# Kernel optimization log

Measured on AMD Instinct MI355X. Metric: run time of the kernel, lower is better.

## Reference

```python
import jax, jax.numpy as jnp
import numpy as np

TWO_PI = 6.283185307179586
ALPHA_CLIP = 0.999

def setup_inputs() -> dict:
    key = jax.random.key(0)
    k1, k2, k3, k4 = jax.random.split(key, 4)
    N, H, W = 256, 512, 512
    xyz = jax.random.uniform(k1, (N, 2), jnp.float32, -1.0, 1.0)      # NDC centers in [-1,1]
    rotation = jax.random.normal(k2, (N, 1), jnp.float32)             # pre-sigmoid angle
    scaling = jax.random.uniform(k3, (N, 2), jnp.float32, 0.05, 0.5)  # inverse std (init 1/5)
    features_dc = jax.random.uniform(k4, (N, 3), jnp.float32)         # RGB in [0,1]
    opacity = jnp.ones((N, 1), jnp.float32)                            # buffer of ones
    background = jnp.ones((3,), jnp.float32)                           # white background
    return {"xyz": xyz, "rotation": rotation, "scaling": scaling,
            "features_dc": features_dc, "opacity": opacity,
            "background": background, "H": H, "W": W}

def _render(xyz, rotation, scaling, features_dc, opacity, background, H, W):
    N = xyz.shape[0]
    # Project NDC [-1,1] -> pixel coords (x,y)
    wh = jnp.array([W, H], jnp.float32)
    means = (xyz * 0.5 + 0.5) * wh                                    # [N,2]
    # Anisotropic 2D covariance: std = 1/|scaling| px, angle via sigmoid
    theta = jax.nn.sigmoid(rotation[:, 0]) * TWO_PI                   # [N]
    std = 1.0 / (jnp.abs(scaling) + 1e-6)                             # [N,2]
    s0, s1 = std[:, 0] ** 2, std[:, 1] ** 2
    c, s = jnp.cos(theta), jnp.sin(theta)
    # Sigma = R diag(s0,s1) R^T
    A = c * c * s0 + s * s * s1
    B = c * s * (s0 - s1)
    Cc = s * s * s0 + c * c * s1
    det = A * Cc - B * B + 1e-12
    ia, ib, ic = Cc / det, -B / det, A / det                          # conic (inverse cov)
    # Pixel centers, flattened P = H*W
    px = jnp.arange(W, dtype=jnp.float32) + 0.5
    py = jnp.arange(H, dtype=jnp.float32) + 0.5
    gx, gy = jnp.meshgrid(px, py)                                     # [H,W]
    gx, gy = gx.reshape(-1), gy.reshape(-1)                           # [P]
    dx = gx[None, :] - means[:, 0:1]                                  # [N,P]
    dy = gy[None, :] - means[:, 1:2]                                  # [N,P]
    power = -0.5 * (ia[:, None] * dx * dx + 2.0 * ib[:, None] * dx * dy
                    + ic[:, None] * dy * dy)                          # [N,P] <= 0
    alpha = jnp.minimum(opacity * jnp.exp(power), ALPHA_CLIP)         # [N,P]
    # Front-to-back alpha compositing in gaussian index order
    logs = jnp.log1p(-alpha)                                          # [N,P]
    csum = jnp.cumsum(logs, axis=0)
    T_excl = jnp.exp(jnp.concatenate([jnp.zeros((1, alpha.shape[1]), alpha.dtype),
                                      csum[:-1]], axis=0))            # transmittance before i
    weights = alpha * T_excl                                          # [N,P]
    T_final = jnp.exp(csum[-1])                                       # [P]
    img = jnp.einsum('np,nc->cp', weights, features_dc)               # [3,P]
    img = img + background[:, None] * T_final[None, :]
    return img.reshape(3, H, W)

def reference(xyz, rotation, scaling, features_dc, opacity, background, H, W):
    return _render(xyz, rotation, scaling, features_dc, opacity, background, H, W)
```

## Files before the change

### kernel.cpp

```cpp
#include <hip/hip_runtime.h>
#include <math.h>


#define BLOCK 256
#define QMAX 30.0f
#define ALPHA_CLIP 0.999f
#define LOG2E 1.4426950408889634f

__global__ __launch_bounds__(BLOCK) void render_kernel(
    const float* __restrict__ xyz,
    const float* __restrict__ rot,
    const float* __restrict__ scal,
    const float* __restrict__ feat,
    const float* __restrict__ opac,
    const float* __restrict__ bg,
    const int* __restrict__ dH,
    const int* __restrict__ dW,
    float* __restrict__ out,
    int N, int P)
{
    __shared__ float sg[BLOCK * 16];
    __shared__ int   list[BLOCK];
    __shared__ int   wcnt[BLOCK / 64];
    __shared__ int   sM;

    const int t = threadIdx.x;
    const int W = *dW, H = *dH;
    const int tiles_x = W >> 6;
    const int tx0 = (blockIdx.x % tiles_x) << 6;
    const int ty0 = (blockIdx.x / tiles_x) << 4;

    const float fx0 = (float)tx0, fx1 = (float)(tx0 + 64);
    const float fy0 = (float)ty0, fy1 = (float)(ty0 + 16);

    const float gxp  = fx0 + (float)(t & 63) + 0.5f;
    const float gyp0 = fy0 + (float)(t >> 6) + 0.5f;

    float T[4]  = {1.f, 1.f, 1.f, 1.f};
    float ar[4] = {0.f, 0.f, 0.f, 0.f};
    float ag[4] = {0.f, 0.f, 0.f, 0.f};
    float ab[4] = {0.f, 0.f, 0.f, 0.f};

    for (int c0 = 0; c0 < N; c0 += BLOCK) {
        const int i = c0 + t;
        bool pred = false;
        if (i < N) {
            const float Wf = (float)W, Hf = (float)H;
            const float mx = (xyz[2*i]   * 0.5f + 0.5f) * Wf;
            const float my = (xyz[2*i+1] * 0.5f + 0.5f) * Hf;
            const float r  = rot[i];
            const float theta = (1.0f / (1.0f + expf(-r))) * 6.283185307179586f;
            const float sd0 = 1.0f / (fabsf(scal[2*i])   + 1e-6f);
            const float sd1 = 1.0f / (fabsf(scal[2*i+1]) + 1e-6f);
            const float s0 = sd0 * sd0, s1 = sd1 * sd1;
            const float c = cosf(theta), s = sinf(theta);
            const float A  = c*c*s0 + s*s*s1;
            const float B  = c*s*(s0 - s1);
            const float Cc = s*s*s0 + c*c*s1;
            const float det = A*Cc - B*B + 1e-12f;
            const float inv = 1.0f / det;
            const float kk = -0.5f * LOG2E;
            const float rx = sqrtf(QMAX * A);
            const float ry = sqrtf(QMAX * Cc);

            float* rec = &sg[t * 16];
            rec[0]  = mx;
            rec[1]  = my;
            rec[2]  = Cc * inv * kk;
            rec[3]  = -B * inv * 2.0f * kk;
            rec[4]  = A  * inv * kk;
            rec[5]  = log2f(opac[i]);
            rec[6]  = feat[3*i+0];
            rec[7]  = feat[3*i+1];
            rec[8]  = feat[3*i+2];
            rec[12] = mx - rx;
            rec[13] = mx + rx;
            rec[14] = my - ry;
            rec[15] = my + ry;

            pred = (rec[13] >= fx0) & (rec[12] <= fx1) &
                   (rec[15] >= fy0) & (rec[14] <= fy1);
        }

        const unsigned long long m = __ballot(pred);
        const int lane = t & 63, wid = t >> 6;
        if (lane == 0) wcnt[wid] = __popcll(m);
        __syncthreads();
        int off = 0;
        for (int w = 0; w < wid; ++w) off += wcnt[w];
        if (pred)
            list[off + __popcll(m & ((1ull << lane) - 1ull))] = t;
        if (t == 0) sM = wcnt[0] + wcnt[1] + wcnt[2] + wcnt[3];
        __syncthreads();
        const int M = sM;

        for (int j = 0; j < M; ++j) {
            const int idx = list[j];
            const float* rec = &sg[idx * 16];
            const float4 g0 = *(const float4*)rec;
            const float4 g1 = *(const float4*)(rec + 4);
            const float  cb = rec[8];
            const float dx = gxp - g0.x;
            const float q0 = fmaf(g0.z * dx, dx, g1.y);
            const float bx = g0.w * dx;
#pragma unroll
            for (int k = 0; k < 4; ++k) {
                const float dy = (gyp0 + 4.0f * (float)k) - g0.y;
                const float ea = fmaf(dy, fmaf(g1.x, dy, bx), q0);
                const float alpha = fminf(exp2f(ea), ALPHA_CLIP);
                const float w = alpha * T[k];
                ar[k] = fmaf(w, g1.z, ar[k]);
                ag[k] = fmaf(w, g1.w, ag[k]);
                ab[k] = fmaf(w, cb, ab[k]);
                T[k] -= w;
            }
        }
        __syncthreads();
    }

    const float b0 = bg[0], b1 = bg[1], b2 = bg[2];
    const int px = tx0 + (t & 63);
#pragma unroll
    for (int k = 0; k < 4; ++k) {
        const int py = ty0 + (t >> 6) + 4 * k;
        if (px < W && py < H) {
            const int p = py * W + px;
            out[p]         = fmaf(b0, T[k], ar[k]);
            out[P + p]     = fmaf(b1, T[k], ag[k]);
            out[2*P + p]   = fmaf(b2, T[k], ab[k]);
        }
    }
}

extern "C" void kernel_launch(void* const* d_in, const int* in_sizes, int n_in,
                              void* d_out, int out_size, void* d_ws, size_t ws_size,
                              hipStream_t stream) {
    const float* xyz  = (const float*)d_in[0];
    const float* rot  = (const float*)d_in[1];
    const float* scal = (const float*)d_in[2];
    const float* feat = (const float*)d_in[3];
    const float* opac = (const float*)d_in[4];
    const float* bg   = (const float*)d_in[5];
    const int*   dH   = (const int*)d_in[6];
    const int*   dW   = (const int*)d_in[7];
    float* out = (float*)d_out;

    const int N = in_sizes[0] / 2;
    const int P = out_size / 3;

    const int blocks = (P + 1023) / 1024;
    render_kernel<<<blocks, BLOCK, 0, stream>>>(xyz, rot, scal, feat, opac, bg,
                                                dH, dW, out, N, P);
}
```

Measured before the change: 72.26 us.

## Precompute gaussian records in a prep kernel and halve tile size

Moves per-gaussian parameter setup (sigmoid, sin/cos, conic, bounding box) into a separate prep kernel that writes 16-float records to workspace, so each render block only loads them with float4 reads instead of recomputing them. It also shrinks the pixel tile from 64x16 to 32x16, which doubles the block count and gives each thread 2 pixels instead of 4. The goal is less redundant transcendental math per block and more blocks to fill the GPU, at the cost of an extra kernel launch and less per-thread reuse of each gaussian load.

```diff
diff --git a/kernel.cpp b/kernel.cpp
--- a/kernel.cpp
+++ b/kernel.cpp
@@ -7,14 +7,53 @@
 #define ALPHA_CLIP 0.999f
 #define LOG2E 1.4426950408889634f
 
+__global__ void prep_kernel(const float* __restrict__ xyz,
+                            const float* __restrict__ rot,
+                            const float* __restrict__ scal,
+                            const float* __restrict__ feat,
+                            const float* __restrict__ opac,
+                            const int* __restrict__ dH,
+                            const int* __restrict__ dW,
+                            float* __restrict__ gp, int N) {
+    int i = blockIdx.x * blockDim.x + threadIdx.x;
+    if (i >= N) return;
+    const float Wf = (float)(*dW), Hf = (float)(*dH);
+    const float mx = (xyz[2*i]   * 0.5f + 0.5f) * Wf;
+    const float my = (xyz[2*i+1] * 0.5f + 0.5f) * Hf;
+    const float r  = rot[i];
+    const float theta = (1.0f / (1.0f + expf(-r))) * 6.283185307179586f;
+    const float sd0 = 1.0f / (fabsf(scal[2*i])   + 1e-6f);
+    const float sd1 = 1.0f / (fabsf(scal[2*i+1]) + 1e-6f);
+    const float s0 = sd0 * sd0, s1 = sd1 * sd1;
+    const float c = cosf(theta), s = sinf(theta);
+    const float A  = c*c*s0 + s*s*s1;
+    const float B  = c*s*(s0 - s1);
+    const float Cc = s*s*s0 + c*c*s1;
+    const float det = A*Cc - B*B + 1e-12f;
+    const float inv = 1.0f / det;
+    const float kk = -0.5f * LOG2E;
+    const float rx = sqrtf(QMAX * A);
+    const float ry = sqrtf(QMAX * Cc);
+    float* rec = &gp[i * 16];
+    rec[0]  = mx;
+    rec[1]  = my;
+    rec[2]  = Cc * inv * kk;
+    rec[3]  = -B * inv * 2.0f * kk;
+    rec[4]  = A  * inv * kk;
+    rec[5]  = log2f(opac[i]);
+    rec[6]  = feat[3*i+0];
+    rec[7]  = feat[3*i+1];
+    rec[8]  = feat[3*i+2];
+    rec[9]  = 0.f; rec[10] = 0.f; rec[11] = 0.f;
+    rec[12] = mx - rx;
+    rec[13] = mx + rx;
+    rec[14] = my - ry;
+    rec[15] = my + ry;
+}
+
 __global__ __launch_bounds__(BLOCK) void render_kernel(
-    const float* __restrict__ xyz,
-    const float* __restrict__ rot,
-    const float* __restrict__ scal,
-    const float* __restrict__ feat,
-    const float* __restrict__ opac,
+    const float* __restrict__ gp,
     const float* __restrict__ bg,
-    const int* __restrict__ dH,
     const int* __restrict__ dW,
     float* __restrict__ out,
     int N, int P)
@@ -25,61 +64,30 @@
     __shared__ int   sM;
 
     const int t = threadIdx.x;
-    const int W = *dW, H = *dH;
-    const int tiles_x = W >> 6;
-    const int tx0 = (blockIdx.x % tiles_x) << 6;
+    const int W = *dW;
+    const int tiles_x = W >> 5;
+    const int tx0 = (blockIdx.x % tiles_x) << 5;
     const int ty0 = (blockIdx.x / tiles_x) << 4;
 
-    const float fx0 = (float)tx0, fx1 = (float)(tx0 + 64);
+    const float fx0 = (float)tx0, fx1 = (float)(tx0 + 32);
     const float fy0 = (float)ty0, fy1 = (float)(ty0 + 16);
 
-    const float gxp  = fx0 + (float)(t & 63) + 0.5f;
-    const float gyp0 = fy0 + (float)(t >> 6) + 0.5f;
+    const float gxp  = fx0 + (float)(t & 31) + 0.5f;
+    const float gyp0 = fy0 + (float)(t >> 5) + 0.5f;
 
-    float T[4]  = {1.f, 1.f, 1.f, 1.f};
-    float ar[4] = {0.f, 0.f, 0.f, 0.f};
-    float ag[4] = {0.f, 0.f, 0.f, 0.f};
-    float ab[4] = {0.f, 0.f, 0.f, 0.f};
+    float T[2]  = {1.f, 1.f};
+    float ar[2] = {0.f, 0.f}, ag[2] = {0.f, 0.f}, ab[2] = {0.f, 0.f};
 
     for (int c0 = 0; c0 < N; c0 += BLOCK) {
         const int i = c0 + t;
         bool pred = false;
         if (i < N) {
-            const float Wf = (float)W, Hf = (float)H;
-            const float mx = (xyz[2*i]   * 0.5f + 0.5f) * Wf;
-            const float my = (xyz[2*i+1] * 0.5f + 0.5f) * Hf;
-            const float r  = rot[i];
-            const float theta = (1.0f / (1.0f + expf(-r))) * 6.283185307179586f;
-            const float sd0 = 1.0f / (fabsf(scal[2*i])   + 1e-6f);
-            const float sd1 = 1.0f / (fabsf(scal[2*i+1]) + 1e-6f);
-            const float s0 = sd0 * sd0, s1 = sd1 * sd1;
-            const float c = cosf(theta), s = sinf(theta);
-            const float A  = c*c*s0 + s*s*s1;
-            const float B  = c*s*(s0 - s1);
-            const float Cc = s*s*s0 + c*c*s1;
-            const float det = A*Cc - B*B + 1e-12f;
-            const float inv = 1.0f / det;
-            const float kk = -0.5f * LOG2E;
-            const float rx = sqrtf(QMAX * A);
-            const float ry = sqrtf(QMAX * Cc);
-
-            float* rec = &sg[t * 16];
-            rec[0]  = mx;
-            rec[1]  = my;
-            rec[2]  = Cc * inv * kk;
-            rec[3]  = -B * inv * 2.0f * kk;
-            rec[4]  = A  * inv * kk;
-            rec[5]  = log2f(opac[i]);
-            rec[6]  = feat[3*i+0];
-            rec[7]  = feat[3*i+1];
-            rec[8]  = feat[3*i+2];
-            rec[12] = mx - rx;
-            rec[13] = mx + rx;
-            rec[14] = my - ry;
-            rec[15] = my + ry;
-
-            pred = (rec[13] >= fx0) & (rec[12] <= fx1) &
-                   (rec[15] >= fy0) & (rec[14] <= fy1);
+            const float4* src = (const float4*)&gp[i * 16];
+            float4 r0 = src[0], r1 = src[1], r2 = src[2], r3 = src[3];
+            float4* dst = (float4*)&sg[t * 16];
+            dst[0] = r0; dst[1] = r1; dst[2] = r2; dst[3] = r3;
+            pred = (r3.y >= fx0) & (r3.x <= fx1) &
+                   (r3.w >= fy0) & (r3.z <= fy1);
         }
 
         const unsigned long long m = __ballot(pred);
@@ -95,8 +103,7 @@
         const int M = sM;
 
         for (int j = 0; j < M; ++j) {
-            const int idx = list[j];
-            const float* rec = &sg[idx * 16];
+            const float* rec = &sg[list[j] * 16];
             const float4 g0 = *(const float4*)rec;
             const float4 g1 = *(const float4*)(rec + 4);
             const float  cb = rec[8];
@@ -104,8 +111,8 @@
             const float q0 = fmaf(g0.z * dx, dx, g1.y);
             const float bx = g0.w * dx;
 #pragma unroll
-            for (int k = 0; k < 4; ++k) {
-                const float dy = (gyp0 + 4.0f * (float)k) - g0.y;
+            for (int k = 0; k < 2; ++k) {
+                const float dy = (gyp0 + 8.0f * (float)k) - g0.y;
                 const float ea = fmaf(dy, fmaf(g1.x, dy, bx), q0);
                 const float alpha = fminf(exp2f(ea), ALPHA_CLIP);
                 const float w = alpha * T[k];
@@ -119,12 +126,12 @@
     }
 
     const float b0 = bg[0], b1 = bg[1], b2 = bg[2];
-    const int px = tx0 + (t & 63);
+    const int px = tx0 + (t & 31);
 #pragma unroll
-    for (int k = 0; k < 4; ++k) {
-        const int py = ty0 + (t >> 6) + 4 * k;
-        if (px < W && py < H) {
-            const int p = py * W + px;
+    for (int k = 0; k < 2; ++k) {
+        const int py = ty0 + (t >> 5) + 8 * k;
+        const int p = py * W + px;
+        if (p < P) {
             out[p]         = fmaf(b0, T[k], ar[k]);
             out[P + p]     = fmaf(b1, T[k], ag[k]);
             out[2*P + p]   = fmaf(b2, T[k], ab[k]);
@@ -144,11 +151,13 @@
     const int*   dH   = (const int*)d_in[6];
     const int*   dW   = (const int*)d_in[7];
     float* out = (float*)d_out;
+    float* gp  = (float*)d_ws;
 
     const int N = in_sizes[0] / 2;
     const int P = out_size / 3;
 
-    const int blocks = (P + 1023) / 1024;
-    render_kernel<<<blocks, BLOCK, 0, stream>>>(xyz, rot, scal, feat, opac, bg,
-                                                dH, dW, out, N, P);
+    prep_kernel<<<(N + 255) / 256, 256, 0, stream>>>(xyz, rot, scal, feat, opac,
+                                                     dH, dW, gp, N);
+    const int blocks = (P + 511) / 512;
+    render_kernel<<<blocks, BLOCK, 0, stream>>>(gp, bg, dW, out, N, P);
 }
```

After: 73.13 us. Within noise of the previous version (+1.2%).
